# Performance work log

Measured on AMD Instinct MI355X. Metric: run time of the kernel, lower is better.

The kernel has to match this reference:

```python
import jax, jax.numpy as jnp
import numpy as np

K_SIZE = 7
D_MODEL = 128
D_Q = 64
N_HEADS = 4
D_FF = 512
EPS = 1e-5


def _windows(x, k):
    # x: [N,E,H,W] -> [N,E,P,H,W]; zero-padded local k x k windows,
    # row-major over (dy,dx), matching nn.Unfold ordering.
    p = k // 2
    N, E, H, W = x.shape
    xp = jnp.pad(x, ((0, 0), (0, 0), (p, p), (p, p)))
    ws = [xp[:, :, i:i + H, j:j + W] for i in range(k) for j in range(k)]
    return jnp.stack(ws, axis=2)


def _layernorm(x, g, b):
    m = jnp.mean(x, -1, keepdims=True)
    v = jnp.var(x, -1, keepdims=True)
    return (x - m) * jax.lax.rsqrt(v + EPS) * g + b


def setup_inputs() -> dict:
    key = jax.random.key(0)
    ks = jax.random.split(key, 12)
    E, Q, F = D_MODEL, D_Q, D_FF

    def g(k, shape, s=0.02):
        return jax.random.normal(k, shape, jnp.float32) * s

    return dict(
        x=jax.random.normal(ks[0], (4, E, 64, 64), jnp.float32),
        qcoeff=jax.random.normal(ks[1], (4, Q), jnp.float32),
        wq=g(ks[2], (E, E)), bq=jnp.zeros((E,), jnp.float32),
        wk=g(ks[3], (E, E)), bk=jnp.zeros((E,), jnp.float32),
        wv=g(ks[4], (E, E)), bv=jnp.zeros((E,), jnp.float32),
        rel_bias=jnp.zeros((N_HEADS, K_SIZE * K_SIZE), jnp.float32),
        ln1_g=jnp.ones((E,), jnp.float32), ln1_b=jnp.zeros((E,), jnp.float32),
        bil_w=g(ks[5], (E, E, Q)), bil_b=jnp.zeros((E,), jnp.float32),
        ln2_g=jnp.ones((E,), jnp.float32), ln2_b=jnp.zeros((E,), jnp.float32),
        w1=g(ks[6], (F, E)), b1=jnp.zeros((F,), jnp.float32),
        w2=g(ks[7], (E, F)), b2=jnp.zeros((E,), jnp.float32),
    )


def reference(x, qcoeff, wq, bq, wk, bk, wv, bv, rel_bias, ln1_g, ln1_b,
              bil_w, bil_b, ln2_g, ln2_b, w1, b1, w2, b2):
    N, E, H, W = x.shape
    Nh = N_HEADS
    Hd = E // Nh
    P = K_SIZE * K_SIZE

    x_nhwc = jnp.transpose(x, (0, 2, 3, 1))              # [N,H,W,E]
    xn = _layernorm(x_nhwc, ln1_g, ln1_b)
    xnc = jnp.transpose(xn, (0, 3, 1, 2))                # [N,E,H,W]

    # 1x1-conv projections
    q = jnp.einsum('nchw,oc->nohw', xnc, wq) + bq[None, :, None, None]
    k = jnp.einsum('nchw,oc->nohw', xnc, wk) + bk[None, :, None, None]
    v = jnp.einsum('nchw,oc->nohw', xnc, wv) + bv[None, :, None, None]

    # local windows of K/V: [N,Nh,Hd,P,H,W]
    Kw = _windows(k, K_SIZE).reshape(N, Nh, Hd, P, H, W)
    Vw = _windows(v, K_SIZE).reshape(N, Nh, Hd, P, H, W)
    Qh = q.reshape(N, Nh, Hd, H, W)

    scores = jnp.einsum('nhdyx,nhdpyx->nhpyx', Qh, Kw)
    scores = scores + rel_bias[None, :, :, None, None]
    attn = jax.nn.softmax(scores, axis=2)                # softmax over P
    out = jnp.einsum('nhpyx,nhdpyx->nhdyx', attn, Vw).reshape(N, E, H, W)
    z0 = jnp.transpose(out, (0, 2, 3, 1))                # [N,H,W,E]

    # Bilinear(z0, qcoeff): qcoeff constant per (H,W) -> contract once per batch
    t = jnp.einsum('oiq,nq->noi', bil_w, qcoeff)         # [N,E,E]
    z1 = jnp.einsum('nhwi,noi->nhwo', z0, t) + bil_b

    z2 = z1 + x_nhwc
    z3 = _layernorm(z2, ln2_g, ln2_b)
    h1 = jax.nn.gelu(z3 @ w1.T + b1, approximate=False)  # dropout inactive (eval)
    z4 = h1 @ w2.T + b2 + z2
    return jnp.transpose(z4, (0, 3, 1, 2))               # [N,E,H,W]
```

## Files before the change

kernel.cpp:

```cpp
#include <hip/hip_runtime.h>
#include <cmath>

#define EPS 1e-5f
#define SZ 2097152

typedef __attribute__((ext_vector_type(8))) short short8;
typedef __attribute__((ext_vector_type(4))) float floatx4;

__device__ __forceinline__ float dot4(float4 a, float4 b) {
  return fmaf(a.x, b.x, fmaf(a.y, b.y, fmaf(a.z, b.z, a.w * b.w)));
}

__device__ __forceinline__ short f2bf(float f) {
  union { float f; unsigned u; } v; v.f = f;
  unsigned r = v.u + 0x7fff + ((v.u >> 16) & 1);
  return (short)(r >> 16);
}

#define MFMA16(a, b, c) __builtin_amdgcn_mfma_f32_16x16x32_bf16(a, b, c, 0, 0, 0)

__global__ __launch_bounds__(256) void k_prep(const float* __restrict__ w1,
    const float* __restrict__ w2, const float* __restrict__ wq,
    const float* __restrict__ wk, const float* __restrict__ wv,
    const float* __restrict__ bil_w, const float* __restrict__ qcoeff,
    short* __restrict__ w1bf, short* __restrict__ w2bf,
    short* __restrict__ wqbf, short* __restrict__ wkbf, short* __restrict__ wvbf,
    short* __restrict__ tb) {
  __shared__ float qs[256];
  int tid = threadIdx.x;
  qs[tid] = qcoeff[tid];
  __syncthreads();
  int tid0 = blockIdx.x * 256 + tid;
  int stride = gridDim.x * 256;
  for (int i = tid0; i < 16384; i += stride) {
    int flat = i * 4; int f = flat >> 7, c = flat & 127;
    float4 v = *(const float4*)&w1[flat];
    short t4[4] = {f2bf(v.x), f2bf(v.y), f2bf(v.z), f2bf(v.w)};
    *(uint2*)&w1bf[f * 136 + c] = *(uint2*)t4;
  }
  for (int i = tid0; i < 16384; i += stride) {
    int flat = i * 4; int o = flat >> 9, j = flat & 511;
    int ck = j >> 7, jj = j & 127;
    float4 v = *(const float4*)&w2[flat];
    short t4[4] = {f2bf(v.x), f2bf(v.y), f2bf(v.z), f2bf(v.w)};
    *(uint2*)&w2bf[(ck * 128 + o) * 136 + jj] = *(uint2*)t4;
  }
  for (int i = tid0; i < 4096; i += stride) {
    int flat = i * 4; int o = flat >> 7, c = flat & 127;
    float4 a = *(const float4*)&wq[flat];
    float4 b = *(const float4*)&wk[flat];
    float4 cc = *(const float4*)&wv[flat];
    short ta[4] = {f2bf(a.x), f2bf(a.y), f2bf(a.z), f2bf(a.w)};
    short tb4[4] = {f2bf(b.x), f2bf(b.y), f2bf(b.z), f2bf(b.w)};
    short tc[4] = {f2bf(cc.x), f2bf(cc.y), f2bf(cc.z), f2bf(cc.w)};
    *(uint2*)&wqbf[o * 136 + c] = *(uint2*)ta;
    *(uint2*)&wkbf[o * 136 + c] = *(uint2*)tb4;
    *(uint2*)&wvbf[o * 136 + c] = *(uint2*)tc;
  }
  {
    int flat = tid0;
    const float* wrow = bil_w + (size_t)flat * 64;
    float acc[4] = {0.f, 0.f, 0.f, 0.f};
    for (int qq = 0; qq < 64; qq += 4) {
      float4 w4 = *(const float4*)&wrow[qq];
#pragma unroll
      for (int nn = 0; nn < 4; ++nn) {
        const float* qc = &qs[nn * 64 + qq];
        acc[nn] = fmaf(w4.x, qc[0], fmaf(w4.y, qc[1], fmaf(w4.z, qc[2], fmaf(w4.w, qc[3], acc[nn]))));
      }
    }
    int o = flat >> 7, i = flat & 127;
#pragma unroll
    for (int nn = 0; nn < 4; ++nn) tb[nn * 17408 + o * 136 + i] = f2bf(acc[nn]);
  }
}

__global__ __launch_bounds__(512) void k_qkvln(const float* __restrict__ x,
    const float* __restrict__ g, const float* __restrict__ b,
    const short* __restrict__ wqbf, const short* __restrict__ wkbf,
    const short* __restrict__ wvbf, const float* __restrict__ bq,
    const float* __restrict__ bk, const float* __restrict__ bv,
    float* __restrict__ xnhwc, short* __restrict__ qbf,
    short* __restrict__ kbf, short* __restrict__ vtb) {
  __shared__ float tile[128 * 33];
  __shared__ float mres[32], rres[32];
  __shared__ __align__(16) short xs[32 * 136];
  __shared__ __align__(16) short ws[128 * 136];
  int tid = threadIdx.x;
  int bid = blockIdx.x;
  int half = bid & 1, ny = bid >> 1;
  int n = ny >> 6, y = ny & 63;
  const float* xb = x + (size_t)n * 524288 + y * 64 + half * 32;
  for (int it = 0; it < 8; ++it) {
    int flat = it * 512 + tid;
    int c = flat >> 5, xpl = flat & 31;
    tile[c * 33 + xpl] = xb[(size_t)c * 4096 + xpl];
  }
  __syncthreads();
  {
    int pxl = tid >> 4, cl = tid & 15;
    float s = 0.f, sq = 0.f;
#pragma unroll
    for (int j = 0; j < 8; ++j) {
      float v = tile[(cl * 8 + j) * 33 + pxl];
      s += v; sq += v * v;
    }
    s += __shfl_xor(s, 1);  sq += __shfl_xor(sq, 1);
    s += __shfl_xor(s, 2);  sq += __shfl_xor(sq, 2);
    s += __shfl_xor(s, 4);  sq += __shfl_xor(sq, 4);
    s += __shfl_xor(s, 8);  sq += __shfl_xor(sq, 8);
    if (cl == 0) {
      float m = s * (1.f / 128.f);
      float var = sq * (1.f / 128.f) - m * m;
      mres[pxl] = m;
      rres[pxl] = rsqrtf(var + EPS);
    }
  }
  __syncthreads();
  size_t rowbase = (size_t)ny * 8192 + half * 4096;
  for (int it = 0; it < 8; ++it) {
    int flat = it * 512 + tid;
    int c = flat & 127, pxl = flat >> 7;
    float v = tile[c * 33 + pxl];
    xnhwc[rowbase + flat] = v;
    xs[pxl * 136 + c] = f2bf((v - mres[pxl]) * rres[pxl] * g[c] + b[c]);
  }
  __syncthreads();
  int w = tid >> 6, lane = tid & 63;
  int quad = lane >> 4, r16 = lane & 15;
  int wm = w & 1, wn = w >> 1;
  int stripl = wm * 16;
  short8 a[4];
#pragma unroll
  for (int kk = 0; kk < 4; ++kk)
    a[kk] = *(const short8*)&xs[(stripl + r16) * 136 + kk * 32 + quad * 8];
  const short* wptr[3] = {wqbf, wkbf, wvbf};
  const float* bptr[3] = {bq, bk, bv};
  for (int m = 0; m < 3; ++m) {
    __syncthreads();
    const short* wp = wptr[m];
    for (int i = tid; i < 2176; i += 512)
      *(short8*)&ws[i * 8] = *(const short8*)&wp[i * 8];
    __syncthreads();
    const float* bb = bptr[m];
#pragma unroll
    for (int nt = 0; nt < 2; ++nt) {
      int o0 = wn * 32 + nt * 16;
      floatx4 acc = {0.f, 0.f, 0.f, 0.f};
#pragma unroll
      for (int kk = 0; kk < 4; ++kk) {
        short8 bfr = *(const short8*)&ws[(o0 + r16) * 136 + kk * 32 + quad * 8];
        acc = MFMA16(a[kk], bfr, acc);
      }
      float bv2 = bb[o0 + r16];
      if (m < 2) {
        short* dst = (m == 0) ? qbf : kbf;
#pragma unroll
        for (int r = 0; r < 4; ++r) {
          int pxl = stripl + quad * 4 + r;
          dst[rowbase + pxl * 128 + o0 + r16] = f2bf(acc[r] + bv2);
        }
      } else {
        short t4[4] = {f2bf(acc[0] + bv2), f2bf(acc[1] + bv2),
                       f2bf(acc[2] + bv2), f2bf(acc[3] + bv2)};
        *(uint2*)&vtb[(size_t)(n * 128 + o0 + r16) * 4096 + y * 64 + half * 32 +
                      stripl + quad * 4] = *(uint2*)t4;
      }
    }
  }
}

__global__ __launch_bounds__(1024) void k_at(const short* __restrict__ qbf,
    const short* __restrict__ kbf, const short* __restrict__ vtb,
    const float* __restrict__ rel_bias, const short* __restrict__ tb,
    const float* __restrict__ bil_b, const float* __restrict__ xnhwc,
    const float* __restrict__ g2, const float* __restrict__ b2ln,
    const short* __restrict__ w1bf, const float* __restrict__ b1,
    const short* __restrict__ w2bf, const float* __restrict__ b2,
    float* __restrict__ out) {
  __shared__ __align__(16) char smem[140544];
  short* z3s = (short*)(smem + 89344);
  float* z2s = (float*)(smem + 106752);
  int tid = threadIdx.x;
  int bid = blockIdx.x;
  int n = bid >> 6, y = bid & 63;
  int w16 = tid >> 6, lane = tid & 63;
  int quad = lane >> 4, r16 = lane & 15;
  size_t rowbase = (size_t)bid * 8192;
  int wmE = w16 & 3, wnE = w16 >> 2;
  int stripE = wmE * 16;
  float xres[2][4];
#pragma unroll
  for (int nt = 0; nt < 2; ++nt)
#pragma unroll
    for (int r = 0; r < 4; ++r)
      xres[nt][r] = xnhwc[rowbase + (stripE + quad * 4 + r) * 128 + wnE * 32 + nt * 16 + r16];
  {
    int h = w16 >> 2, sw = w16 & 3;
    int strip = sw * 16;
    float* ssfw = (float*)(smem + w16 * 3200);
    short* Abw = (short*)(smem + 51200 + w16 * 2176);
    float* biasw = (float*)(smem + 86016 + w16 * 208);
    {
      unsigned* ad = (unsigned*)Abw;
      for (int i = lane; i < 544; i += 64) ad[i] = 0u;
    }
    if (lane < 49) biasw[lane] = rel_bias[h * 49 + lane];
    const short* qrow = qbf + (size_t)n * 524288 + (size_t)y * 8192 + h * 32;
    short8 qf = *(const short8*)&qrow[(strip + r16) * 128 + quad * 8];
    const short* kbp = kbf + (size_t)n * 524288 + h * 32;
#pragma unroll
    for (int r = 0; r < 7; ++r) {
      int yy = y + r - 3;
      bool yok = (unsigned)yy < 64u;
      int yyc = min(max(yy, 0), 63);
#pragma unroll
      for (int t = 0; t < 2; ++t) {
        int xxc = (sw + t) * 16 + r16;
        int gx = xxc - 3;
        bool ok = yok && ((unsigned)gx < 64u);
        int gxc = min(max(gx, 0), 63);
        short8 bf = *(const short8*)&kbp[(size_t)(yyc * 64 + gxc) * 128 + quad * 8];
        floatx4 c = MFMA16(qf, bf, ((floatx4){0.f, 0.f, 0.f, 0.f}));
#pragma unroll
        for (int rr = 0; rr < 4; ++rr) {
          int lrow = quad * 4 + rr;
          int dx = xxc - (strip + lrow);
          if ((unsigned)dx < 7u) {
            float val = ok ? c[rr] : 0.f;
            ssfw[lrow * 50 + r * 7 + dx] = val + biasw[r * 7 + dx];
          }
        }
      }
    }
    {
      int lrow = lane >> 2, sub = lane & 3;
      int p0 = sub * 12, cnt = (sub == 3) ? 13 : 12;
      float sv[13];
      float mx = -1e30f;
      for (int pi = 0; pi < cnt; ++pi) { sv[pi] = ssfw[lrow * 50 + p0 + pi]; mx = fmaxf(mx, sv[pi]); }
      mx = fmaxf(mx, __shfl_xor(mx, 1));
      mx = fmaxf(mx, __shfl_xor(mx, 2));
      float sum = 0.f;
      for (int pi = 0; pi < cnt; ++pi) { float e = __expf(sv[pi] - mx); sv[pi] = e; sum += e; }
      sum += __shfl_xor(sum, 1);
      sum += __shfl_xor(sum, 2);
      float inv = 1.f / sum;
      for (int pi = 0; pi < cnt; ++pi) ssfw[lrow * 50 + p0 + pi] = sv[pi] * inv;
    }
    floatx4 oacc[2] = {(floatx4){0.f, 0.f, 0.f, 0.f}, (floatx4){0.f, 0.f, 0.f, 0.f}};
    int kk0 = (sw == 3) ? 1 : 0;
    int kk1 = (sw == 0) ? 0 : 1;
    int lrow = lane >> 2, sub = lane & 3;
    int pxg = strip + lrow;
    const short* vbp = vtb + (size_t)(n * 128 + h * 32) * 4096;
    for (int r = 0; r < 7; ++r) {
      int yy = y + r - 3;
      bool yok = (unsigned)yy < 64u;
      int yyc = min(max(yy, 0), 63);
      int c0 = pxg + sub - 3;
      if ((unsigned)c0 < 64u) Abw[lrow * 68 + c0] = f2bf(ssfw[lrow * 50 + r * 7 + sub]);
      int c1 = pxg + sub + 1;
      if (sub < 3 && (unsigned)c1 < 64u)
        Abw[lrow * 68 + c1] = f2bf(ssfw[lrow * 50 + r * 7 + sub + 4]);
      for (int kk = kk0; kk <= kk1; ++kk) {
        short8 af = *(const short8*)&Abw[r16 * 68 + kk * 32 + quad * 8];
#pragma unroll
        for (int nt = 0; nt < 2; ++nt) {
          short8 vf = *(const short8*)&vbp[(size_t)(nt * 16 + r16) * 4096 + yyc * 64 + kk * 32 + quad * 8];
          if (!yok) vf = (short8){0, 0, 0, 0, 0, 0, 0, 0};
          oacc[nt] = MFMA16(af, vf, oacc[nt]);
        }
      }
    }
#pragma unroll
    for (int nt = 0; nt < 2; ++nt)
#pragma unroll
      for (int rr = 0; rr < 4; ++rr) {
        int px = strip + quad * 4 + rr;
        z3s[px * 136 + h * 32 + nt * 16 + r16] = f2bf(oacc[nt][rr]);
      }
  }
  __syncthreads();
  short* R1s = (short*)smem;
  short* w2c = (short*)(smem + 34816);
  short* h1s = (short*)(smem + 69632);
  float* outt = (float*)smem;
  const short* tn = tb + (size_t)n * 17408;
  for (int i = tid; i < 2176; i += 1024)
    *(short8*)&R1s[i * 8] = *(const short8*)&tn[i * 8];
  __syncthreads();
  int wm = w16 & 3, wn = w16 >> 2;
  int strip = wm * 16;
  {
    short8 a[4];
#pragma unroll
    for (int kk = 0; kk < 4; ++kk)
      a[kk] = *(const short8*)&z3s[(strip + r16) * 136 + kk * 32 + quad * 8];
#pragma unroll
    for (int nt = 0; nt < 2; ++nt) {
      int o0 = wn * 32 + nt * 16;
      floatx4 acc = {0.f, 0.f, 0.f, 0.f};
#pragma unroll
      for (int kk = 0; kk < 4; ++kk) {
        short8 bfr = *(const short8*)&R1s[(o0 + r16) * 136 + kk * 32 + quad * 8];
        acc = MFMA16(a[kk], bfr, acc);
      }
      float bb = bil_b[o0 + r16];
#pragma unroll
      for (int r = 0; r < 4; ++r) {
        int px = strip + quad * 4 + r;
        z2s[px * 132 + o0 + r16] = acc[r] + bb + xres[nt][r];
      }
    }
  }
  __syncthreads();
  {
    int px = tid >> 4, cl = tid & 15;
    float4 v0 = *(const float4*)&z2s[px * 132 + cl * 8];
    float4 v1 = *(const float4*)&z2s[px * 132 + cl * 8 + 4];
    float s = v0.x + v0.y + v0.z + v0.w + v1.x + v1.y + v1.z + v1.w;
    float sq = dot4(v0, v0) + dot4(v1, v1);
    s += __shfl_xor(s, 1);  sq += __shfl_xor(sq, 1);
    s += __shfl_xor(s, 2);  sq += __shfl_xor(sq, 2);
    s += __shfl_xor(s, 4);  sq += __shfl_xor(sq, 4);
    s += __shfl_xor(s, 8);  sq += __shfl_xor(sq, 8);
    float m = s * (1.f / 128.f);
    float var = sq * (1.f / 128.f) - m * m;
    float rr = rsqrtf(var + EPS);
    int c0 = cl * 8;
    short t8[8];
#pragma unroll
    for (int j = 0; j < 8; ++j) {
      float vv = (j < 4) ? (&v0.x)[j] : (&v1.x)[j - 4];
      t8[j] = f2bf((vv - m) * rr * g2[c0 + j] + b2ln[c0 + j]);
    }
    *(uint4*)&z3s[px * 136 + c0] = *(uint4*)t8;
  }
  __syncthreads();
  short8 a3[4];
#pragma unroll
  for (int kk = 0; kk < 4; ++kk)
    a3[kk] = *(const short8*)&z3s[(strip + r16) * 136 + kk * 32 + quad * 8];
  floatx4 zacc[2];
  zacc[0] = (floatx4){0.f, 0.f, 0.f, 0.f};
  zacc[1] = (floatx4){0.f, 0.f, 0.f, 0.f};
  for (int fc = 0; fc < 512; fc += 128) {
    __syncthreads();
    const short* w1src = w1bf + fc * 136;
    const short* w2src = w2bf + (fc >> 7) * 17408;
    for (int i = tid; i < 2176; i += 1024) {
      *(short8*)&R1s[i * 8] = *(const short8*)&w1src[i * 8];
      *(short8*)&w2c[i * 8] = *(const short8*)&w2src[i * 8];
    }
    __syncthreads();
#pragma unroll
    for (int nt = 0; nt < 2; ++nt) {
      int f0 = wn * 32 + nt * 16;
      floatx4 acc = {0.f, 0.f, 0.f, 0.f};
#pragma unroll
      for (int kk = 0; kk < 4; ++kk) {
        short8 bfr = *(const short8*)&R1s[(f0 + r16) * 136 + kk * 32 + quad * 8];
        acc = MFMA16(a3[kk], bfr, acc);
      }
      float bb1 = b1[fc + f0 + r16];
#pragma unroll
      for (int r = 0; r < 4; ++r) {
        float hv = acc[r] + bb1;
        float ge = 0.5f * hv * (1.f + erff(hv * 0.70710678118f));
        h1s[(strip + quad * 4 + r) * 136 + f0 + r16] = f2bf(ge);
      }
    }
    __syncthreads();
    short8 ah[4];
#pragma unroll
    for (int kk = 0; kk < 4; ++kk)
      ah[kk] = *(const short8*)&h1s[(strip + r16) * 136 + kk * 32 + quad * 8];
#pragma unroll
    for (int nt = 0; nt < 2; ++nt) {
      int o0 = wn * 32 + nt * 16;
#pragma unroll
      for (int kk = 0; kk < 4; ++kk) {
        short8 bfr = *(const short8*)&w2c[(o0 + r16) * 136 + kk * 32 + quad * 8];
        zacc[nt] = MFMA16(ah[kk], bfr, zacc[nt]);
      }
    }
  }
  __syncthreads();
#pragma unroll
  for (int nt = 0; nt < 2; ++nt) {
    int o0 = wn * 32 + nt * 16;
    float bb = b2[o0 + r16];
#pragma unroll
    for (int r = 0; r < 4; ++r) {
      int px = strip + quad * 4 + r;
      outt[(o0 + r16) * 65 + px] = zacc[nt][r] + bb + z2s[px * 132 + o0 + r16];
    }
  }
  __syncthreads();
  for (int it = 0; it < 8; ++it) {
    int flat = it * 1024 + tid;
    int o = flat >> 6, px = flat & 63;
    out[(((size_t)(n * 128 + o)) * 64 + y) * 64 + px] = outt[o * 65 + px];
  }
}

extern "C" void kernel_launch(void* const* d_in, const int* in_sizes, int n_in,
                              void* d_out, int out_size, void* d_ws, size_t ws_size,
                              hipStream_t stream) {
  const float* x        = (const float*)d_in[0];
  const float* qcoeff   = (const float*)d_in[1];
  const float* wq       = (const float*)d_in[2];
  const float* bq       = (const float*)d_in[3];
  const float* wk       = (const float*)d_in[4];
  const float* bk       = (const float*)d_in[5];
  const float* wv       = (const float*)d_in[6];
  const float* bv       = (const float*)d_in[7];
  const float* rel_bias = (const float*)d_in[8];
  const float* ln1_g    = (const float*)d_in[9];
  const float* ln1_b    = (const float*)d_in[10];
  const float* bil_w    = (const float*)d_in[11];
  const float* bil_b    = (const float*)d_in[12];
  const float* ln2_g    = (const float*)d_in[13];
  const float* ln2_b    = (const float*)d_in[14];
  const float* w1       = (const float*)d_in[15];
  const float* b1       = (const float*)d_in[16];
  const float* w2       = (const float*)d_in[17];
  const float* b2       = (const float*)d_in[18];
  float* out = (float*)d_out;

  float* ws = (float*)d_ws;
  float* x_nhwc = ws;
  short* qbf = (short*)(ws + 2 * SZ);
  short* kbf = qbf + SZ;
  short* vtb = kbf + SZ;
  short* bf     = (short*)(ws + 4 * SZ);
  short* tb     = bf;
  short* w1bf   = bf + 4 * 17408;
  short* w2bf   = w1bf + 512 * 136;
  short* wqbf   = w2bf + 4 * 17408;
  short* wkbf   = wqbf + 17408;
  short* wvbf   = wkbf + 17408;

  k_prep<<<64, 256, 0, stream>>>(w1, w2, wq, wk, wv, bil_w, qcoeff,
                                 w1bf, w2bf, wqbf, wkbf, wvbf, tb);
  k_qkvln<<<512, 512, 0, stream>>>(x, ln1_g, ln1_b, wqbf, wkbf, wvbf,
                                   bq, bk, bv, x_nhwc, qbf, kbf, vtb);
  k_at<<<256, 1024, 0, stream>>>(qbf, kbf, vtb, rel_bias, tb, bil_b, x_nhwc,
                                 ln2_g, ln2_b, w1bf, b1, w2bf, b2, out);
}
```

Baseline: 148.9 us.

## Split attention-MLP kernel into half-row blocks and read weights directly from global

Splits each image row across two 512-thread blocks, which halves shared memory per block and doubles the grid. This should allow more resident blocks per CU and better spread over the 256 CUs. Weight tiles for the bilinear, W1 and W2 GEMMs are no longer staged in LDS; MFMA B fragments are read straight from global/L2, which also drops several block-wide barriers. The output transpose through LDS is replaced by direct float4 stores, and the softmax loops are fully unrolled. The trade-off is more global load traffic and latency on the weight fragments.

Measured after the change: 153.9 us. +3.3%, slower.

```diff
diff --git a/kernel.cpp b/kernel.cpp
--- a/kernel.cpp
+++ b/kernel.cpp
@@ -170,7 +170,7 @@
   }
 }
 
-__global__ __launch_bounds__(1024) void k_at(const short* __restrict__ qbf,
+__global__ __launch_bounds__(512, 4) void k_at(const short* __restrict__ qbf,
     const short* __restrict__ kbf, const short* __restrict__ vtb,
     const float* __restrict__ rel_bias, const short* __restrict__ tb,
     const float* __restrict__ bil_b, const float* __restrict__ xnhwc,
@@ -178,29 +178,33 @@
     const short* __restrict__ w1bf, const float* __restrict__ b1,
     const short* __restrict__ w2bf, const float* __restrict__ b2,
     float* __restrict__ out) {
-  __shared__ __align__(16) char smem[140544];
-  short* z3s = (short*)(smem + 89344);
-  float* z2s = (float*)(smem + 106752);
+  __shared__ __align__(16) char smem[70272];
+  short* h1s = (short*)smem;
+  short* z3s = (short*)(smem + 44672);
+  float* z2s = (float*)(smem + 53376);
   int tid = threadIdx.x;
   int bid = blockIdx.x;
-  int n = bid >> 6, y = bid & 63;
+  int half = bid & 1, ny = bid >> 1;
+  int n = ny >> 6, y = ny & 63;
   int w16 = tid >> 6, lane = tid & 63;
   int quad = lane >> 4, r16 = lane & 15;
-  size_t rowbase = (size_t)bid * 8192;
-  int wmE = w16 & 3, wnE = w16 >> 2;
-  int stripE = wmE * 16;
+  size_t rowbase = (size_t)ny * 8192;
+  int wm = w16 & 1, wn = w16 >> 1;
+  int stripL = wm * 16;
   float xres[2][4];
 #pragma unroll
   for (int nt = 0; nt < 2; ++nt)
 #pragma unroll
     for (int r = 0; r < 4; ++r)
-      xres[nt][r] = xnhwc[rowbase + (stripE + quad * 4 + r) * 128 + wnE * 32 + nt * 16 + r16];
+      xres[nt][r] = xnhwc[rowbase + (half * 32 + stripL + quad * 4 + r) * 128 +
+                          wn * 32 + nt * 16 + r16];
   {
-    int h = w16 >> 2, sw = w16 & 3;
-    int strip = sw * 16;
+    int h = w16 >> 1, swl = w16 & 1;
+    int sg = half * 2 + swl;
+    int strip = sg * 16;
     float* ssfw = (float*)(smem + w16 * 3200);
-    short* Abw = (short*)(smem + 51200 + w16 * 2176);
-    float* biasw = (float*)(smem + 86016 + w16 * 208);
+    short* Abw = (short*)(smem + 25600 + w16 * 2176);
+    float* biasw = (float*)(smem + 43008 + w16 * 208);
     {
       unsigned* ad = (unsigned*)Abw;
       for (int i = lane; i < 544; i += 64) ad[i] = 0u;
@@ -216,7 +220,7 @@
       int yyc = min(max(yy, 0), 63);
 #pragma unroll
       for (int t = 0; t < 2; ++t) {
-        int xxc = (sw + t) * 16 + r16;
+        int xxc = (sg + t) * 16 + r16;
         int gx = xxc - 3;
         bool ok = yok && ((unsigned)gx < 64u);
         int gxc = min(max(gx, 0), 63);
@@ -235,22 +239,33 @@
     }
     {
       int lrow = lane >> 2, sub = lane & 3;
-      int p0 = sub * 12, cnt = (sub == 3) ? 13 : 12;
+      int p0 = sub * 12;
       float sv[13];
       float mx = -1e30f;
-      for (int pi = 0; pi < cnt; ++pi) { sv[pi] = ssfw[lrow * 50 + p0 + pi]; mx = fmaxf(mx, sv[pi]); }
+#pragma unroll
+      for (int pi = 0; pi < 13; ++pi) {
+        sv[pi] = ssfw[lrow * 50 + p0 + pi];
+        mx = fmaxf(mx, sv[pi]);
+      }
       mx = fmaxf(mx, __shfl_xor(mx, 1));
       mx = fmaxf(mx, __shfl_xor(mx, 2));
       float sum = 0.f;
-      for (int pi = 0; pi < cnt; ++pi) { float e = __expf(sv[pi] - mx); sv[pi] = e; sum += e; }
+#pragma unroll
+      for (int pi = 0; pi < 13; ++pi) {
+        float e = __expf(sv[pi] - mx);
+        if (pi == 12 && sub != 3) e = 0.f;
+        sv[pi] = e; sum += e;
+      }
       sum += __shfl_xor(sum, 1);
       sum += __shfl_xor(sum, 2);
       float inv = 1.f / sum;
-      for (int pi = 0; pi < cnt; ++pi) ssfw[lrow * 50 + p0 + pi] = sv[pi] * inv;
+#pragma unroll
+      for (int pi = 0; pi < 13; ++pi)
+        if (pi < 12 || sub == 3) ssfw[lrow * 50 + p0 + pi] = sv[pi] * inv;
     }
     floatx4 oacc[2] = {(floatx4){0.f, 0.f, 0.f, 0.f}, (floatx4){0.f, 0.f, 0.f, 0.f}};
-    int kk0 = (sw == 3) ? 1 : 0;
-    int kk1 = (sw == 0) ? 0 : 1;
+    int kk0 = (sg == 3) ? 1 : 0;
+    int kk1 = (sg == 0) ? 0 : 1;
     int lrow = lane >> 2, sub = lane & 3;
     int pxg = strip + lrow;
     const short* vbp = vtb + (size_t)(n * 128 + h * 32) * 4096;
@@ -277,40 +292,31 @@
     for (int nt = 0; nt < 2; ++nt)
 #pragma unroll
       for (int rr = 0; rr < 4; ++rr) {
-        int px = strip + quad * 4 + rr;
-        z3s[px * 136 + h * 32 + nt * 16 + r16] = f2bf(oacc[nt][rr]);
-      }
-  }
-  __syncthreads();
-  short* R1s = (short*)smem;
-  short* w2c = (short*)(smem + 34816);
-  short* h1s = (short*)(smem + 69632);
-  float* outt = (float*)smem;
-  const short* tn = tb + (size_t)n * 17408;
-  for (int i = tid; i < 2176; i += 1024)
-    *(short8*)&R1s[i * 8] = *(const short8*)&tn[i * 8];
-  __syncthreads();
-  int wm = w16 & 3, wn = w16 >> 2;
-  int strip = wm * 16;
+        int pxl = swl * 16 + quad * 4 + rr;
+        z3s[pxl * 136 + h * 32 + nt * 16 + r16] = f2bf(oacc[nt][rr]);
+      }
+  }
+  __syncthreads();
   {
+    const short* tn = tb + (size_t)n * 17408;
     short8 a[4];
 #pragma unroll
     for (int kk = 0; kk < 4; ++kk)
-      a[kk] = *(const short8*)&z3s[(strip + r16) * 136 + kk * 32 + quad * 8];
+      a[kk] = *(const short8*)&z3s[(stripL + r16) * 136 + kk * 32 + quad * 8];
 #pragma unroll
     for (int nt = 0; nt < 2; ++nt) {
       int o0 = wn * 32 + nt * 16;
       floatx4 acc = {0.f, 0.f, 0.f, 0.f};
 #pragma unroll
       for (int kk = 0; kk < 4; ++kk) {
-        short8 bfr = *(const short8*)&R1s[(o0 + r16) * 136 + kk * 32 + quad * 8];
+        short8 bfr = *(const short8*)&tn[(o0 + r16) * 136 + kk * 32 + quad * 8];
         acc = MFMA16(a[kk], bfr, acc);
       }
       float bb = bil_b[o0 + r16];
 #pragma unroll
       for (int r = 0; r < 4; ++r) {
-        int px = strip + quad * 4 + r;
-        z2s[px * 132 + o0 + r16] = acc[r] + bb + xres[nt][r];
+        int pxl = stripL + quad * 4 + r;
+        z2s[pxl * 132 + o0 + r16] = acc[r] + bb + xres[nt][r];
       }
     }
   }
@@ -341,26 +347,18 @@
   short8 a3[4];
 #pragma unroll
   for (int kk = 0; kk < 4; ++kk)
-    a3[kk] = *(const short8*)&z3s[(strip + r16) * 136 + kk * 32 + quad * 8];
+    a3[kk] = *(const short8*)&z3s[(stripL + r16) * 136 + kk * 32 + quad * 8];
   floatx4 zacc[2];
   zacc[0] = (floatx4){0.f, 0.f, 0.f, 0.f};
   zacc[1] = (floatx4){0.f, 0.f, 0.f, 0.f};
   for (int fc = 0; fc < 512; fc += 128) {
-    __syncthreads();
-    const short* w1src = w1bf + fc * 136;
-    const short* w2src = w2bf + (fc >> 7) * 17408;
-    for (int i = tid; i < 2176; i += 1024) {
-      *(short8*)&R1s[i * 8] = *(const short8*)&w1src[i * 8];
-      *(short8*)&w2c[i * 8] = *(const short8*)&w2src[i * 8];
-    }
-    __syncthreads();
 #pragma unroll
     for (int nt = 0; nt < 2; ++nt) {
       int f0 = wn * 32 + nt * 16;
       floatx4 acc = {0.f, 0.f, 0.f, 0.f};
 #pragma unroll
       for (int kk = 0; kk < 4; ++kk) {
-        short8 bfr = *(const short8*)&R1s[(f0 + r16) * 136 + kk * 32 + quad * 8];
+        short8 bfr = *(const short8*)&w1bf[(fc + f0 + r16) * 136 + kk * 32 + quad * 8];
         acc = MFMA16(a3[kk], bfr, acc);
       }
       float bb1 = b1[fc + f0 + r16];
@@ -368,40 +366,36 @@
       for (int r = 0; r < 4; ++r) {
         float hv = acc[r] + bb1;
         float ge = 0.5f * hv * (1.f + erff(hv * 0.70710678118f));
-        h1s[(strip + quad * 4 + r) * 136 + f0 + r16] = f2bf(ge);
+        h1s[(stripL + quad * 4 + r) * 136 + f0 + r16] = f2bf(ge);
       }
     }
     __syncthreads();
     short8 ah[4];
 #pragma unroll
     for (int kk = 0; kk < 4; ++kk)
-      ah[kk] = *(const short8*)&h1s[(strip + r16) * 136 + kk * 32 + quad * 8];
+      ah[kk] = *(const short8*)&h1s[(stripL + r16) * 136 + kk * 32 + quad * 8];
+    const short* w2src = w2bf + (fc >> 7) * 17408;
 #pragma unroll
     for (int nt = 0; nt < 2; ++nt) {
       int o0 = wn * 32 + nt * 16;
 #pragma unroll
       for (int kk = 0; kk < 4; ++kk) {
-        short8 bfr = *(const short8*)&w2c[(o0 + r16) * 136 + kk * 32 + quad * 8];
+        short8 bfr = *(const short8*)&w2src[(o0 + r16) * 136 + kk * 32 + quad * 8];
         zacc[nt] = MFMA16(ah[kk], bfr, zacc[nt]);
       }
     }
-  }
-  __syncthreads();
+    __syncthreads();
+  }
 #pragma unroll
   for (int nt = 0; nt < 2; ++nt) {
-    int o0 = wn * 32 + nt * 16;
-    float bb = b2[o0 + r16];
-#pragma unroll
-    for (int r = 0; r < 4; ++r) {
-      int px = strip + quad * 4 + r;
-      outt[(o0 + r16) * 65 + px] = zacc[nt][r] + bb + z2s[px * 132 + o0 + r16];
-    }
-  }
-  __syncthreads();
-  for (int it = 0; it < 8; ++it) {
-    int flat = it * 1024 + tid;
-    int o = flat >> 6, px = flat & 63;
-    out[(((size_t)(n * 128 + o)) * 64 + y) * 64 + px] = outt[o * 65 + px];
+    int o = wn * 32 + nt * 16 + r16;
+    float bb = b2[o];
+    float res[4];
+#pragma unroll
+    for (int r = 0; r < 4; ++r)
+      res[r] = zacc[nt][r] + bb + z2s[(stripL + quad * 4 + r) * 132 + o];
+    *(float4*)&out[(((size_t)(n * 128 + o)) * 64 + y) * 64 + half * 32 + stripL + quad * 4] =
+        *(float4*)res;
   }
 }
 
@@ -446,6 +440,6 @@
                                  w1bf, w2bf, wqbf, wkbf, wvbf, tb);
   k_qkvln<<<512, 512, 0, stream>>>(x, ln1_g, ln1_b, wqbf, wkbf, wvbf,
                                    bq, bk, bv, x_nhwc, qbf, kbf, vtb);
-  k_at<<<256, 1024, 0, stream>>>(qbf, kbf, vtb, rel_bias, tb, bil_b, x_nhwc,
-                                 ln2_g, ln2_b, w1bf, b1, w2bf, b2, out);
-}
+  k_at<<<512, 512, 0, stream>>>(qbf, kbf, vtb, rel_bias, tb, bil_b, x_nhwc,
+                                ln2_g, ln2_b, w1bf, b1, w2bf, b2, out);
+}
```
